# Performance work log

Hardware: AMD Instinct MI355X
Metric: run time of the kernel (lower is better)

Reference implementation:

```python
import jax, jax.numpy as jnp
import numpy as np

B, S, D, H = 2, 2048, 1024, 16
DK = D // H  # 64
THETA = 10000.0


def setup_inputs() -> dict:
    key = jax.random.key(0)
    ks = jax.random.split(key, 5)
    std = float(np.sqrt(2.0 / (D + D)))
    x = jax.random.normal(ks[0], (B, S, D), dtype=jnp.float32)
    q_proj = jax.random.normal(ks[1], (D, D), dtype=jnp.float32) * std
    k_proj = jax.random.normal(ks[2], (D, D), dtype=jnp.float32) * std
    v_proj = jax.random.normal(ks[3], (D, D), dtype=jnp.float32) * std
    o_proj = jax.random.normal(ks[4], (D, D), dtype=jnp.float32) * std
    token_positions = jnp.arange(S, dtype=jnp.int32).reshape(1, S)
    return {"x": x, "token_positions": token_positions,
            "q_proj": q_proj, "k_proj": k_proj, "v_proj": v_proj, "o_proj": o_proj}


def _rope(t, pos):
    # t: [B, H, S, DK]; pos: [S]. Equivalent to multiplying by the block-diagonal
    # rotation matrix R[pos] in the source (interleaved 2x2 rotations).
    inv_freq = 1.0 / (THETA ** (2.0 * jnp.arange(DK // 2, dtype=jnp.float32) / DK))
    ang = pos.astype(jnp.float32)[:, None] * inv_freq[None, :]  # [S, DK/2]
    c, s = jnp.cos(ang), jnp.sin(ang)
    t0, t1 = t[..., 0::2], t[..., 1::2]
    out0 = c * t0 - s * t1
    out1 = s * t0 + c * t1
    return jnp.stack([out0, out1], axis=-1).reshape(t.shape)


def reference(x, token_positions, q_proj, k_proj, v_proj, o_proj):
    def split_heads(t):  # [B,S,D] -> [B,H,S,DK]
        return t.reshape(B, S, H, DK).transpose(0, 2, 1, 3)

    q = split_heads(jnp.einsum('bsd,ed->bse', x, q_proj))
    k = split_heads(jnp.einsum('bsd,ed->bse', x, k_proj))
    v = split_heads(jnp.einsum('bsd,ed->bse', x, v_proj))

    pos = token_positions[0]
    q = _rope(q, pos)
    k = _rope(k, pos)

    scores = jnp.einsum('bhqd,bhkd->bhqk', q, k) / jnp.sqrt(jnp.float32(DK))
    causal = jnp.tril(jnp.ones((S, S), dtype=bool))
    scores = jnp.where(causal, scores, -jnp.inf)

    # Faithful to source softmax: subtract the GLOBAL max (x.max()), then row-normalize.
    p = jnp.exp(scores - jnp.max(scores))
    p = p / jnp.sum(p, axis=-1, keepdims=True)

    attn = jnp.einsum('bhqk,bhkd->bhqd', p, v)
    attn = attn.transpose(0, 2, 1, 3).reshape(B, S, D)  # merge heads
    return jnp.einsum('bsd,ed->bse', attn, o_proj)
```

## Files before the change

kernel.cpp:

```cpp
#include <hip/hip_runtime.h>
#include <math.h>

#define B_  2
#define S_  2048
#define D_  1024
#define H_  16
#define DK_ 64
#define M_  (B_ * S_)

using u16 = unsigned short;
using u32 = unsigned int;
typedef __attribute__((ext_vector_type(8))) short  short8;
typedef __attribute__((ext_vector_type(4))) short  short4v;
typedef __attribute__((ext_vector_type(4))) float  float4v;
typedef __attribute__((ext_vector_type(4))) float  f32x4;
typedef __attribute__((ext_vector_type(4))) u32    u32x4;

__device__ __forceinline__ float bf2f(u16 h) {
  u32 u = ((u32)h) << 16;
  return __builtin_bit_cast(float, u);
}
__device__ __forceinline__ u16 f2bf(float f) {
  u32 u = __builtin_bit_cast(u32, f);
  u32 r = u + 0x7fffu + ((u >> 16) & 1u);
  return (u16)(r >> 16);
}

__device__ __forceinline__ void async16(const void* g, void* l) {
  __builtin_amdgcn_global_load_lds((const __attribute__((address_space(1))) void*)g,
                                   (__attribute__((address_space(3))) void*)l,
                                   16, 0, 0);
}

#define MFMA16(a, b, c) __builtin_amdgcn_mfma_f32_16x16x32_bf16((a), (b), (c), 0, 0, 0)

__device__ __forceinline__ void stc(u16* p, float v)   { *p = f2bf(v); }
__device__ __forceinline__ void stc(float* p, float v) { *p = v; }

#define XG_ (M_ * D_ / 4)
#define WG_ (D_ * D_ / 4)
__global__ __launch_bounds__(256) void cvt5_kernel(
    const float* __restrict__ x,  const float* __restrict__ wq,
    const float* __restrict__ wk, const float* __restrict__ wv,
    const float* __restrict__ wo, u16* __restrict__ Xb, u16* __restrict__ Wqb,
    u16* __restrict__ Wkb, u16* __restrict__ Wvb, u16* __restrict__ Wob) {
  int i = blockIdx.x * 256 + threadIdx.x;
  const float* s; u16* d; int off;
  if (i < XG_)                { s = x;  d = Xb;  off = i; }
  else if (i < XG_ + WG_)     { s = wq; d = Wqb; off = i - XG_; }
  else if (i < XG_ + 2 * WG_) { s = wk; d = Wkb; off = i - XG_ - WG_; }
  else if (i < XG_ + 3 * WG_) { s = wv; d = Wvb; off = i - XG_ - 2 * WG_; }
  else                        { s = wo; d = Wob; off = i - XG_ - 3 * WG_; }
  f32x4 v = ((const f32x4*)s)[off];
  short4v o;
  o[0] = (short)f2bf(v[0]); o[1] = (short)f2bf(v[1]);
  o[2] = (short)f2bf(v[2]); o[3] = (short)f2bf(v[3]);
  ((short4v*)d)[off] = o;
}

template <typename TC>
__device__ __forceinline__ void gemm_tile(const u16* __restrict__ A,
                                          const u16* __restrict__ Bw,
                                          TC* __restrict__ C,
                                          int K, int N, int m0, int n0) {
  __shared__ __align__(16) u16 As[128 * 32];
  __shared__ __align__(16) u16 Bs[128 * 32];
  const int tid  = threadIdx.x;
  const int lane = tid & 63;
  const int wave = tid >> 6;
  const int quad = lane >> 4;
  const int l15  = lane & 15;
  const int wm   = (wave >> 1) << 6;
  const int wn   = (wave & 1) << 6;

  float4v acc[4][4];
#pragma unroll
  for (int i = 0; i < 4; ++i)
#pragma unroll
    for (int j = 0; j < 4; ++j) acc[i][j] = (float4v){0.f, 0.f, 0.f, 0.f};

  for (int k0 = 0; k0 < K; k0 += 32) {
#pragma unroll
    for (int i = 0; i < 2; ++i) {
      const int cbase = i * 256 + wave * 64;
      const int c     = cbase + lane;
      async16(A  + (size_t)(m0 + (c >> 2)) * K + k0 + ((c & 3) << 3), As + cbase * 8);
      async16(Bw + (size_t)(n0 + (c >> 2)) * K + k0 + ((c & 3) << 3), Bs + cbase * 8);
    }
    __syncthreads();

    short8 af[4], bfr[4];
#pragma unroll
    for (int mi = 0; mi < 4; ++mi)
      af[mi] = *(const short8*)(As + (wm + mi * 16 + l15) * 32 + quad * 8);
#pragma unroll
    for (int ni = 0; ni < 4; ++ni)
      bfr[ni] = *(const short8*)(Bs + (wn + ni * 16 + l15) * 32 + quad * 8);
#pragma unroll
    for (int mi = 0; mi < 4; ++mi)
#pragma unroll
      for (int ni = 0; ni < 4; ++ni)
        acc[mi][ni] = MFMA16(af[mi], bfr[ni], acc[mi][ni]);
    __syncthreads();
  }

#pragma unroll
  for (int mi = 0; mi < 4; ++mi)
#pragma unroll
    for (int ni = 0; ni < 4; ++ni)
#pragma unroll
      for (int r = 0; r < 4; ++r) {
        const int row = m0 + wm + mi * 16 + quad * 4 + r;
        const int col = n0 + wn + ni * 16 + l15;
        stc(C + (size_t)row * N + col, acc[mi][ni][r]);
      }
}

__global__ __launch_bounds__(256) void gemm_qkv_kernel(
    const u16* __restrict__ X, const u16* __restrict__ Wq,
    const u16* __restrict__ Wk, const u16* __restrict__ Wv,
    u16* Qb, u16* Kb, u16* Vb) {
  const int mt  = blockIdx.x;
  const int nn  = blockIdx.y;
  const int sel = nn >> 3;
  const int nt  = nn & 7;
  const u16* Bw = (sel == 0) ? Wq : (sel == 1) ? Wk : Wv;
  u16*       C  = (sel == 0) ? Qb : (sel == 1) ? Kb : Vb;
  gemm_tile(X, Bw, C, D_, D_, mt * 128, nt * 128);
}

__global__ __launch_bounds__(256) void gemm_o_kernel(
    const u16* __restrict__ Ab, const u16* __restrict__ Wo, float* Out) {
  gemm_tile(Ab, Wo, Out, D_, D_, blockIdx.x * 128, blockIdx.y * 128);
}

__global__ __launch_bounds__(256) void rope_kernel(u16* __restrict__ Qb,
                                                   u16* __restrict__ Kb,
                                                   const void* __restrict__ posv) {
  const int tid = threadIdx.x;
  const int t  = blockIdx.x * 256 + tid;
  const int p4 = t & 7;
  const int h  = (t >> 3) & (H_ - 1);
  const int s  = (t >> 7) & (S_ - 1);
  const int b  = t >> 18;
  __shared__ float tabc[2][32], tabs[2][32];
  const int* p32 = (const int*)posv;
  const bool is64 = (p32[1] == 0 && p32[2] == 1);
  if (tid < 64) {
    const int sl = tid >> 5, i = tid & 31;
    const int sg = ((blockIdx.x * 2) & (S_ - 1)) + sl;
    const int ps = is64 ? p32[2 * sg] : p32[sg];
    const float freq = exp2f(-0.4152410118609203f * (float)i);
    float sn, cs;
    sincosf((float)ps * freq, &sn, &cs);
    tabc[sl][i] = cs; tabs[sl][i] = sn;
  }
  __syncthreads();
  const int sl = (tid >> 7) & 1;
  const size_t base = (size_t)(b * S_ + s) * D_ + h * DK_ + p4 * 8;
  short8 qv = *(const short8*)(Qb + base);
  short8 kv = *(const short8*)(Kb + base);
  short8 qo, ko;
#pragma unroll
  for (int j = 0; j < 4; ++j) {
    const int i = p4 * 4 + j;
    const float cs = tabc[sl][i], sn = tabs[sl][i];
    const float q0v = bf2f((u16)qv[2 * j]), q1v = bf2f((u16)qv[2 * j + 1]);
    qo[2 * j]     = (short)f2bf(0.125f * (cs * q0v - sn * q1v));
    qo[2 * j + 1] = (short)f2bf(0.125f * (sn * q0v + cs * q1v));
    const float k0v = bf2f((u16)kv[2 * j]), k1v = bf2f((u16)kv[2 * j + 1]);
    ko[2 * j]     = (short)f2bf(cs * k0v - sn * k1v);
    ko[2 * j + 1] = (short)f2bf(sn * k0v + cs * k1v);
  }
  *(short8*)(Qb + base) = qo;
  *(short8*)(Kb + base) = ko;
}

__global__ __launch_bounds__(256) void vtrans_kernel(const u16* __restrict__ Vb,
                                                     u16* __restrict__ Vt) {
  const int sblk = blockIdx.x;
  const int bh   = blockIdx.y;
  const int b = bh >> 4, h = bh & 15;
  const int t = threadIdx.x;
  const int s0 = sblk * 64;
  __shared__ __align__(16) u16 T[64 * 72];

  {
    const int srow = t >> 2;
    const int dseg = (t & 3) << 4;
    const u16* g = Vb + (size_t)(b * S_ + s0 + srow) * D_ + h * DK_ + dseg;
    *(short8*)(T + srow * 72 + dseg)     = *(const short8*)(g);
    *(short8*)(T + srow * 72 + dseg + 8) = *(const short8*)(g + 8);
  }
  __syncthreads();
  {
    const int dk   = t >> 2;
    const int sseg = (t & 3) << 4;
    short8 o0, o1;
#pragma unroll
    for (int jj = 0; jj < 8; ++jj) {
      const int ss0 = sseg + jj;
      const int ss1 = sseg + 8 + jj;
      const int k0l = (((ss0 & 31) >> 3) << 2) + (((ss0 >> 2) & 1) << 4) +
                      (ss0 & 3) + (ss0 & 32);
      const int k1l = (((ss1 & 31) >> 3) << 2) + (((ss1 >> 2) & 1) << 4) +
                      (ss1 & 3) + (ss1 & 32);
      o0[jj] = (short)T[k0l * 72 + dk];
      o1[jj] = (short)T[k1l * 72 + dk];
    }
    u16* g = Vt + (size_t)(bh * DK_ + dk) * S_ + s0 + sseg;
    *(short8*)(g)     = o0;
    *(short8*)(g + 8) = o1;
  }
}

__global__ __launch_bounds__(256, 4) void attn_kernel(const u16* __restrict__ Qb,
                                                      const u16* __restrict__ Kb,
                                                      const u16* __restrict__ Vt,
                                                      u16* __restrict__ Ob) {
  const int j5 = (blockIdx.x + blockIdx.y) & 31;
  const int r5 = j5 & 7, g5 = j5 >> 3;
  const int qt = (g5 == 0) ? r5 : (g5 == 1) ? r5 + 8 : (g5 == 2) ? 23 - r5 : 31 - r5;
  const int bh = blockIdx.y;
  const int b = bh >> 4, h = bh & 15;
  const int tid = threadIdx.x, lane = tid & 63, wave = tid >> 6;
  const int qh = wave >> 1, kh = wave & 1;
  const int quad = lane >> 4, l15 = lane & 15;
  const int qw = qt * 64 + qh * 32;

  __shared__ __align__(16) u16 SM[2][2][64 * 64];

  const char* kp = (const char*)(Kb + (size_t)b * S_ * D_ + h * DK_);
  const char* vp = (const char*)(Vt + (size_t)bh * DK_ * S_);

  int koffb[2], voffb[2];
#pragma unroll
  for (int i = 0; i < 2; ++i) {
    const int c  = wave * 128 + i * 64 + lane;
    const int kr = c >> 3;
    const int kj = (c & 7) ^ (kr & 7);
    koffb[i] = kr * (D_ * 2) + kj * 16;
    const int vdk = c >> 3;
    const int vj  = (c & 7) ^ (vdk & 7);
    voffb[i] = vdk * (S_ * 2) + vj * 16;
  }

  auto stage = [&](int sel) {
#pragma unroll
    for (int i = 0; i < 2; ++i) {
      const int cb = wave * 128 + i * 64;
      async16(kp + koffb[i], &SM[0][sel][cb * 8]);
      async16(vp + voffb[i], &SM[1][sel][cb * 8]);
    }
    kp += 64 * D_ * 2;
    vp += 128;
  };

  const int x7   = l15 & 7;
  const int krd0 = (kh * 32 + l15) * 64 + ((quad ^ x7) << 3);
  const int krd1 = (kh * 32 + l15) * 64 + (((quad + 4) ^ x7) << 3);
  const int vrd  = l15 * 64 + (((kh * 4 + quad) ^ x7) << 3);

  short8 qf[2][2];
#pragma unroll
  for (int rg = 0; rg < 2; ++rg) {
    const u16* qrow = Qb + (size_t)(b * S_ + qw + rg * 16 + l15) * D_ + h * DK_;
    qf[rg][0] = *(const short8*)(qrow + quad * 8);
    qf[rg][1] = *(const short8*)(qrow + 32 + quad * 8);
  }

  short8 ones;
#pragma unroll
  for (int j = 0; j < 8; ++j) ones[j] = (short)0x3F80;

  float4v oacc[2][4];
#pragma unroll
  for (int rg = 0; rg < 2; ++rg)
#pragma unroll
    for (int n2 = 0; n2 < 4; ++n2) oacc[rg][n2] = (float4v){0.f, 0.f, 0.f, 0.f};
  float4v lacc[2] = {(float4v){0.f, 0.f, 0.f, 0.f}, (float4v){0.f, 0.f, 0.f, 0.f}};

  const int NS = qt + 1;
  stage(0);

  for (int j = 0; j < NS; ++j) {
    asm volatile("s_waitcnt vmcnt(0)" ::: "memory");
    __builtin_amdgcn_s_barrier();
    asm volatile("" ::: "memory");
    if (j + 1 < NS) stage((j + 1) & 1);

    const u16* ks = &SM[0][j & 1][0];
    const u16* vs = &SM[1][j & 1][0];

    float4v sc[2][2];
    __builtin_amdgcn_s_setprio(1);
#pragma unroll
    for (int ni = 0; ni < 2; ++ni) {
      const short8 kf0 = *(const short8*)(ks + krd0 + ni * 1024);
      const short8 kf1 = *(const short8*)(ks + krd1 + ni * 1024);
      float4v z = (float4v){0.f, 0.f, 0.f, 0.f};
      sc[0][ni] = MFMA16(kf1, qf[0][1], MFMA16(kf0, qf[0][0], z));
      sc[1][ni] = MFMA16(kf1, qf[1][1], MFMA16(kf0, qf[1][0], z));
    }
    __builtin_amdgcn_s_setprio(0);

    const int kb = j * 64 + kh * 32;
    if (kb + 31 > qw) {
#pragma unroll
      for (int rg = 0; rg < 2; ++rg) {
        const int qr = qw + rg * 16 + l15;
#pragma unroll
        for (int ni = 0; ni < 2; ++ni)
#pragma unroll
          for (int r = 0; r < 4; ++r) {
            const float e = __expf(sc[rg][ni][r]);
            sc[rg][ni][r] = (kb + ni * 16 + quad * 4 + r > qr) ? 0.f : e;
          }
      }
    } else {
#pragma unroll
      for (int rg = 0; rg < 2; ++rg)
#pragma unroll
        for (int ni = 0; ni < 2; ++ni)
#pragma unroll
          for (int r = 0; r < 4; ++r) sc[rg][ni][r] = __expf(sc[rg][ni][r]);
    }

    short8 pfr[2];
#pragma unroll
    for (int rg = 0; rg < 2; ++rg) {
      u32 w0, w1, w2, w3;
      asm("v_cvt_pk_bf16_f32 %0, %1, %2" : "=v"(w0) : "v"(sc[rg][0][0]), "v"(sc[rg][0][1]));
      asm("v_cvt_pk_bf16_f32 %0, %1, %2" : "=v"(w1) : "v"(sc[rg][0][2]), "v"(sc[rg][0][3]));
      asm("v_cvt_pk_bf16_f32 %0, %1, %2" : "=v"(w2) : "v"(sc[rg][1][0]), "v"(sc[rg][1][1]));
      asm("v_cvt_pk_bf16_f32 %0, %1, %2" : "=v"(w3) : "v"(sc[rg][1][2]), "v"(sc[rg][1][3]));
      u32x4 ww = (u32x4){w0, w1, w2, w3};
      pfr[rg] = __builtin_bit_cast(short8, ww);
    }

    __builtin_amdgcn_s_setprio(1);
    lacc[0] = MFMA16(pfr[0], ones, lacc[0]);
    lacc[1] = MFMA16(pfr[1], ones, lacc[1]);
#pragma unroll
    for (int n2 = 0; n2 < 4; ++n2) {
      const short8 vf = *(const short8*)(vs + vrd + n2 * 1024);
      oacc[0][n2] = MFMA16(pfr[0], vf, oacc[0][n2]);
      oacc[1][n2] = MFMA16(pfr[1], vf, oacc[1][n2]);
    }
    __builtin_amdgcn_s_setprio(0);
  }

  __syncthreads();
  float* comb = (float*)(void*)&SM[0][0][0];
  if (kh == 1) {
    float* cw = comb + (size_t)(qh * 64 + lane) * 41;
#pragma unroll
    for (int rg = 0; rg < 2; ++rg) {
#pragma unroll
      for (int n2 = 0; n2 < 4; ++n2)
#pragma unroll
        for (int r = 0; r < 4; ++r) cw[rg * 16 + n2 * 4 + r] = oacc[rg][n2][r];
#pragma unroll
      for (int r = 0; r < 4; ++r) cw[32 + rg * 4 + r] = lacc[rg][r];
    }
  }
  __syncthreads();
  if (kh == 0) {
    const float* cw = comb + (size_t)(qh * 64 + lane) * 41;
#pragma unroll
    for (int rg = 0; rg < 2; ++rg) {
      float rinv[4];
#pragma unroll
      for (int r = 0; r < 4; ++r)
        rinv[r] = 1.0f / (lacc[rg][r] + cw[32 + rg * 4 + r]);
#pragma unroll
      for (int n2 = 0; n2 < 4; ++n2)
#pragma unroll
        for (int r = 0; r < 4; ++r) {
          const int srow = qw + rg * 16 + quad * 4 + r;
          Ob[(size_t)(b * S_ + srow) * D_ + h * DK_ + n2 * 16 + l15] =
              f2bf((oacc[rg][n2][r] + cw[rg * 16 + n2 * 4 + r]) * rinv[r]);
        }
    }
  }
}

extern "C" void kernel_launch(void* const* d_in, const int* in_sizes, int n_in,
                              void* d_out, int out_size, void* d_ws, size_t ws_size,
                              hipStream_t stream) {
  const float* x  = (const float*)d_in[0];
  const void*  tp = d_in[1];
  const float* wq = (const float*)d_in[2];
  const float* wk = (const float*)d_in[3];
  const float* wv = (const float*)d_in[4];
  const float* wo = (const float*)d_in[5];
  float* out = (float*)d_out;

  u16* Qb  = (u16*)d_ws;
  u16* Kb  = Qb + (size_t)M_ * D_;
  u16* Vb  = Kb + (size_t)M_ * D_;
  u16* Vt  = Vb + (size_t)M_ * D_;
  u16* Ab  = Vt + (size_t)M_ * D_;
  u16* Xb  = Ab;
  u16* Wqb = Ab + (size_t)M_ * D_;
  u16* Wkb = Wqb + (size_t)D_ * D_;
  u16* Wvb = Wkb + (size_t)D_ * D_;
  u16* Wob = Wvb + (size_t)D_ * D_;

  cvt5_kernel<<<dim3((XG_ + 4 * WG_) / 256), dim3(256), 0, stream>>>(
      x, wq, wk, wv, wo, Xb, Wqb, Wkb, Wvb, Wob);
  gemm_qkv_kernel<<<dim3(32, 24), dim3(256), 0, stream>>>(Xb, Wqb, Wkb, Wvb, Qb, Kb, Vb);
  rope_kernel<<<dim3((B_ * S_ * H_ * 8) / 256), dim3(256), 0, stream>>>(Qb, Kb, tp);
  vtrans_kernel<<<dim3(32, 32), dim3(256), 0, stream>>>(Vb, Vt);
  attn_kernel<<<dim3(32, 32), dim3(256), 0, stream>>>(Qb, Kb, Vt, Ab);
  gemm_o_kernel<<<dim3(32, 8), dim3(256), 0, stream>>>(Ab, Wob, out);
}
```

Measured before the change: 180.0 us.

## Fuse RoPE into QK GEMM epilogue and emit transposed V directly

```diff
diff --git a/kernel.cpp b/kernel.cpp
--- a/kernel.cpp
+++ b/kernel.cpp
@@ -34,17 +34,29 @@
 
 #define MFMA16(a, b, c) __builtin_amdgcn_mfma_f32_16x16x32_bf16((a), (b), (c), 0, 0, 0)
 
-__device__ __forceinline__ void stc(u16* p, float v)   { *p = f2bf(v); }
-__device__ __forceinline__ void stc(float* p, float v) { *p = v; }
-
-#define XG_ (M_ * D_ / 4)
-#define WG_ (D_ * D_ / 4)
+#define XG_  (M_ * D_ / 4)
+#define WG_  (D_ * D_ / 4)
+#define TOT_ (XG_ + 4 * WG_)
 __global__ __launch_bounds__(256) void cvt5_kernel(
     const float* __restrict__ x,  const float* __restrict__ wq,
     const float* __restrict__ wk, const float* __restrict__ wv,
     const float* __restrict__ wo, u16* __restrict__ Xb, u16* __restrict__ Wqb,
-    u16* __restrict__ Wkb, u16* __restrict__ Wvb, u16* __restrict__ Wob) {
+    u16* __restrict__ Wkb, u16* __restrict__ Wvb, u16* __restrict__ Wob,
+    float* __restrict__ tab, const void* __restrict__ posv) {
   int i = blockIdx.x * 256 + threadIdx.x;
+  if (i >= TOT_) {
+    const int j  = i - TOT_;
+    const int s  = j >> 5, ii = j & 31;
+    const int* p32 = (const int*)posv;
+    const bool is64 = (p32[1] == 0 && p32[2] == 1);
+    const int  ps   = is64 ? p32[2 * s] : p32[s];
+    const float freq = exp2f(-0.4152410118609203f * (float)ii);
+    float sn, cs;
+    sincosf((float)ps * freq, &sn, &cs);
+    tab[(size_t)j * 2]     = cs;
+    tab[(size_t)j * 2 + 1] = sn;
+    return;
+  }
   const float* s; u16* d; int off;
   if (i < XG_)                { s = x;  d = Xb;  off = i; }
   else if (i < XG_ + WG_)     { s = wq; d = Wqb; off = i - XG_; }
@@ -58,11 +70,12 @@
   ((short4v*)d)[off] = o;
 }
 
-template <typename TC>
+template <int MODE, typename TC>
 __device__ __forceinline__ void gemm_tile(const u16* __restrict__ A,
                                           const u16* __restrict__ Bw,
                                           TC* __restrict__ C,
-                                          int K, int N, int m0, int n0) {
+                                          int K, int N, int m0, int n0,
+                                          const float* __restrict__ tab) {
   __shared__ __align__(16) u16 As[128 * 32];
   __shared__ __align__(16) u16 Bs[128 * 32];
   const int tid  = threadIdx.x;
@@ -104,114 +117,73 @@
     __syncthreads();
   }
 
-#pragma unroll
-  for (int mi = 0; mi < 4; ++mi)
-#pragma unroll
-    for (int ni = 0; ni < 4; ++ni)
+  if constexpr (MODE == 4) {
+#pragma unroll
+    for (int mi = 0; mi < 4; ++mi)
+#pragma unroll
+      for (int ni = 0; ni < 4; ++ni)
+#pragma unroll
+        for (int r = 0; r < 4; ++r) {
+          const int row = m0 + wm + mi * 16 + quad * 4 + r;
+          const int col = n0 + wn + ni * 16 + l15;
+          C[(size_t)row * N + col] = acc[mi][ni][r];
+        }
+  } else if constexpr (MODE == 1 || MODE == 2) {
+    const int p = l15 & 1;
+#pragma unroll
+    for (int mi = 0; mi < 4; ++mi)
 #pragma unroll
       for (int r = 0; r < 4; ++r) {
         const int row = m0 + wm + mi * 16 + quad * 4 + r;
-        const int col = n0 + wn + ni * 16 + l15;
-        stc(C + (size_t)row * N + col, acc[mi][ni][r]);
+        const float* trow = tab + (size_t)(row & (S_ - 1)) * 64;
+#pragma unroll
+        for (int ni = 0; ni < 4; ++ni) {
+          const int ii = ni * 8 + (l15 >> 1);
+          const float cs = trow[2 * ii], sn = trow[2 * ii + 1];
+          const float v  = acc[mi][ni][r];
+          const float pr = __shfl_xor(v, 1, 64);
+          const float t0 = p ? pr : v;
+          const float t1 = p ? v : pr;
+          float o = p ? (sn * t0 + cs * t1) : (cs * t0 - sn * t1);
+          if constexpr (MODE == 1) o *= 0.125f;
+          const int col = n0 + wn + ni * 16 + l15;
+          ((u16*)C)[(size_t)row * N + col] = f2bf(o);
+        }
       }
+  } else {
+#pragma unroll
+    for (int ni = 0; ni < 4; ++ni) {
+      const int col   = n0 + wn + ni * 16 + l15;
+      const int sl    = col & (S_ - 1);
+      const int wslot = ((l15 >> 2) << 3) + ((ni & 1) << 2) + (l15 & 3);
+      const size_t cb = (size_t)(col >> 11) * ((size_t)D_ * S_) +
+                        (size_t)((sl & ~31) + wslot);
+#pragma unroll
+      for (int mi = 0; mi < 4; ++mi)
+#pragma unroll
+        for (int r = 0; r < 4; ++r) {
+          const int e = m0 + wm + mi * 16 + quad * 4 + r;
+          ((u16*)C)[cb + (size_t)e * S_] = f2bf(acc[mi][ni][r]);
+        }
+    }
+  }
 }
 
 __global__ __launch_bounds__(256) void gemm_qkv_kernel(
     const u16* __restrict__ X, const u16* __restrict__ Wq,
     const u16* __restrict__ Wk, const u16* __restrict__ Wv,
-    u16* Qb, u16* Kb, u16* Vb) {
-  const int mt  = blockIdx.x;
+    u16* Qb, u16* Kb, u16* Vt, const float* __restrict__ tab) {
+  const int bx  = blockIdx.x;
   const int nn  = blockIdx.y;
   const int sel = nn >> 3;
-  const int nt  = nn & 7;
-  const u16* Bw = (sel == 0) ? Wq : (sel == 1) ? Wk : Wv;
-  u16*       C  = (sel == 0) ? Qb : (sel == 1) ? Kb : Vb;
-  gemm_tile(X, Bw, C, D_, D_, mt * 128, nt * 128);
+  if (sel == 0)      gemm_tile<1>(X,  Wq, Qb, D_, D_, bx * 128, (nn & 7) * 128, tab);
+  else if (sel == 1) gemm_tile<2>(X,  Wk, Kb, D_, D_, bx * 128, (nn & 7) * 128, tab);
+  else               gemm_tile<3>(Wv, X,  Vt, D_, S_, (nn & 7) * 128, bx * 128, nullptr);
 }
 
 __global__ __launch_bounds__(256) void gemm_o_kernel(
     const u16* __restrict__ Ab, const u16* __restrict__ Wo, float* Out) {
-  gemm_tile(Ab, Wo, Out, D_, D_, blockIdx.x * 128, blockIdx.y * 128);
-}
-
-__global__ __launch_bounds__(256) void rope_kernel(u16* __restrict__ Qb,
-                                                   u16* __restrict__ Kb,
-                                                   const void* __restrict__ posv) {
-  const int tid = threadIdx.x;
-  const int t  = blockIdx.x * 256 + tid;
-  const int p4 = t & 7;
-  const int h  = (t >> 3) & (H_ - 1);
-  const int s  = (t >> 7) & (S_ - 1);
-  const int b  = t >> 18;
-  __shared__ float tabc[2][32], tabs[2][32];
-  const int* p32 = (const int*)posv;
-  const bool is64 = (p32[1] == 0 && p32[2] == 1);
-  if (tid < 64) {
-    const int sl = tid >> 5, i = tid & 31;
-    const int sg = ((blockIdx.x * 2) & (S_ - 1)) + sl;
-    const int ps = is64 ? p32[2 * sg] : p32[sg];
-    const float freq = exp2f(-0.4152410118609203f * (float)i);
-    float sn, cs;
-    sincosf((float)ps * freq, &sn, &cs);
-    tabc[sl][i] = cs; tabs[sl][i] = sn;
-  }
-  __syncthreads();
-  const int sl = (tid >> 7) & 1;
-  const size_t base = (size_t)(b * S_ + s) * D_ + h * DK_ + p4 * 8;
-  short8 qv = *(const short8*)(Qb + base);
-  short8 kv = *(const short8*)(Kb + base);
-  short8 qo, ko;
-#pragma unroll
-  for (int j = 0; j < 4; ++j) {
-    const int i = p4 * 4 + j;
-    const float cs = tabc[sl][i], sn = tabs[sl][i];
-    const float q0v = bf2f((u16)qv[2 * j]), q1v = bf2f((u16)qv[2 * j + 1]);
-    qo[2 * j]     = (short)f2bf(0.125f * (cs * q0v - sn * q1v));
-    qo[2 * j + 1] = (short)f2bf(0.125f * (sn * q0v + cs * q1v));
-    const float k0v = bf2f((u16)kv[2 * j]), k1v = bf2f((u16)kv[2 * j + 1]);
-    ko[2 * j]     = (short)f2bf(cs * k0v - sn * k1v);
-    ko[2 * j + 1] = (short)f2bf(sn * k0v + cs * k1v);
-  }
-  *(short8*)(Qb + base) = qo;
-  *(short8*)(Kb + base) = ko;
-}
-
-__global__ __launch_bounds__(256) void vtrans_kernel(const u16* __restrict__ Vb,
-                                                     u16* __restrict__ Vt) {
-  const int sblk = blockIdx.x;
-  const int bh   = blockIdx.y;
-  const int b = bh >> 4, h = bh & 15;
-  const int t = threadIdx.x;
-  const int s0 = sblk * 64;
-  __shared__ __align__(16) u16 T[64 * 72];
-
-  {
-    const int srow = t >> 2;
-    const int dseg = (t & 3) << 4;
-    const u16* g = Vb + (size_t)(b * S_ + s0 + srow) * D_ + h * DK_ + dseg;
-    *(short8*)(T + srow * 72 + dseg)     = *(const short8*)(g);
-    *(short8*)(T + srow * 72 + dseg + 8) = *(const short8*)(g + 8);
-  }
-  __syncthreads();
-  {
-    const int dk   = t >> 2;
-    const int sseg = (t & 3) << 4;
-    short8 o0, o1;
-#pragma unroll
-    for (int jj = 0; jj < 8; ++jj) {
-      const int ss0 = sseg + jj;
-      const int ss1 = sseg + 8 + jj;
-      const int k0l = (((ss0 & 31) >> 3) << 2) + (((ss0 >> 2) & 1) << 4) +
-                      (ss0 & 3) + (ss0 & 32);
-      const int k1l = (((ss1 & 31) >> 3) << 2) + (((ss1 >> 2) & 1) << 4) +
-                      (ss1 & 3) + (ss1 & 32);
-      o0[jj] = (short)T[k0l * 72 + dk];
-      o1[jj] = (short)T[k1l * 72 + dk];
-    }
-    u16* g = Vt + (size_t)(bh * DK_ + dk) * S_ + s0 + sseg;
-    *(short8*)(g)     = o0;
-    *(short8*)(g + 8) = o1;
-  }
+  gemm_tile<4>(Ab, Wo, Out, D_, D_, blockIdx.x * 128, blockIdx.y * 128, nullptr);
 }
 
 __global__ __launch_bounds__(256, 4) void attn_kernel(const u16* __restrict__ Qb,
@@ -398,20 +370,19 @@
 
   u16* Qb  = (u16*)d_ws;
   u16* Kb  = Qb + (size_t)M_ * D_;
-  u16* Vb  = Kb + (size_t)M_ * D_;
-  u16* Vt  = Vb + (size_t)M_ * D_;
+  u16* Vt  = Kb + (size_t)M_ * D_;
   u16* Ab  = Vt + (size_t)M_ * D_;
   u16* Xb  = Ab;
   u16* Wqb = Ab + (size_t)M_ * D_;
   u16* Wkb = Wqb + (size_t)D_ * D_;
   u16* Wvb = Wkb + (size_t)D_ * D_;
   u16* Wob = Wvb + (size_t)D_ * D_;
-
-  cvt5_kernel<<<dim3((XG_ + 4 * WG_) / 256), dim3(256), 0, stream>>>(
-      x, wq, wk, wv, wo, Xb, Wqb, Wkb, Wvb, Wob);
-  gemm_qkv_kernel<<<dim3(32, 24), dim3(256), 0, stream>>>(Xb, Wqb, Wkb, Wvb, Qb, Kb, Vb);
-  rope_kernel<<<dim3((B_ * S_ * H_ * 8) / 256), dim3(256), 0, stream>>>(Qb, Kb, tp);
-  vtrans_kernel<<<dim3(32, 32), dim3(256), 0, stream>>>(Vb, Vt);
+  float* tab = (float*)(Wob + (size_t)D_ * D_);
+
+  cvt5_kernel<<<dim3((TOT_ + 65536) / 256), dim3(256), 0, stream>>>(
+      x, wq, wk, wv, wo, Xb, Wqb, Wkb, Wvb, Wob, tab, tp);
+  gemm_qkv_kernel<<<dim3(32, 24), dim3(256), 0, stream>>>(Xb, Wqb, Wkb, Wvb,
+                                                          Qb, Kb, Vt, tab);
   attn_kernel<<<dim3(32, 32), dim3(256), 0, stream>>>(Qb, Kb, Vt, Ab);
   gemm_o_kernel<<<dim3(32, 8), dim3(256), 0, stream>>>(Ab, Wob, out);
 }
```

Result: no change. 182.0 us (+1.1%).
